# Kernel tuning notes

Measured on AMD Instinct MI355X. Metric: run time of the kernel, lower is better.

The kernel has to match this reference:

```python
import jax, jax.numpy as jnp
import numpy as np

BN_EPS = 1e-5
DIST_EPS = 1e-8
K = 3  # fixed 3-NN interpolation


def _cond_conv(x, t_embed, w_t, b_t, w_c, b_c, gamma, beta):
    # time conditioning: GELU(t) -> Linear -> add to channels
    te = jax.nn.gelu(t_embed, approximate=False) @ w_t.T + b_t  # (B, Cin)
    x = x + te[:, :, None]
    # kernel-size-1 Conv1d == channel GEMM
    x = jnp.einsum('oc,bcn->bon', w_c, x) + b_c[None, :, None]
    # BatchNorm1d, training mode: biased stats over (batch, length)
    m = jnp.mean(x, axis=(0, 2), keepdims=True)
    v = jnp.var(x, axis=(0, 2), keepdims=True)
    x = gamma[None, :, None] * (x - m) * jax.lax.rsqrt(v + BN_EPS) + beta[None, :, None]
    return jax.nn.gelu(x, approximate=False)


def _forward(xyz1, xyz2, points1, points2, t_embed,
             w_t1, b_t1, w_c1, b_c1, g1, be1,
             w_t2, b_t2, w_c2, b_c2, g2, be2):
    # squared euclidean distances (cdist**2), computed directly
    # d2[b,n,s] = ||xyz1[b,n]||^2 + ||xyz2[b,s]||^2 - 2 <xyz1[b,n], xyz2[b,s]>
    n1 = jnp.sum(xyz1 * xyz1, axis=-1)  # (B,N)
    n2 = jnp.sum(xyz2 * xyz2, axis=-1)  # (B,S)
    d2 = n1[:, :, None] + n2[:, None, :] - 2.0 * jnp.einsum('bnc,bsc->bns', xyz1, xyz2)
    # top-3 smallest distances (instead of wasteful full sort)
    neg, idx = jax.lax.top_k(-d2, K)        # (B,N,3)
    dists = -neg
    dist_recip = 1.0 / (dists + DIST_EPS)
    weight = dist_recip / jnp.sum(dist_recip, axis=2, keepdims=True)  # (B,N,3)
    pts2t = jnp.transpose(points2, (0, 2, 1))  # (B,S,C2)
    gathered = jax.vmap(lambda p, i: p[i])(pts2t, idx)  # (B,N,3,C2)
    interp = jnp.einsum('bnkc,bnk->bcn', gathered, weight)  # (B,C2,N)
    new_points = jnp.concatenate([points1, interp], axis=1)  # (B,C1+C2,N)
    new_points = _cond_conv(new_points, t_embed, w_t1, b_t1, w_c1, b_c1, g1, be1)
    new_points = _cond_conv(new_points, t_embed, w_t2, b_t2, w_c2, b_c2, g2, be2)
    return new_points


def setup_inputs() -> dict:
    key = jax.random.key(0)
    ks = jax.random.split(key, 12)
    B, N, S, C1, C2, T = 8, 8192, 2048, 128, 256, 256
    Cin = C1 + C2
    s = lambda fan: 1.0 / np.sqrt(fan)
    return {
        'xyz1': jax.random.normal(ks[0], (B, N, 3), jnp.float32),
        'xyz2': jax.random.normal(ks[1], (B, S, 3), jnp.float32),
        'points1': jax.random.normal(ks[2], (B, C1, N), jnp.float32),
        'points2': jax.random.normal(ks[3], (B, C2, S), jnp.float32),
        't_embed': jax.random.normal(ks[4], (B, T), jnp.float32),
        'w_t1': jax.random.normal(ks[5], (Cin, T), jnp.float32) * s(T),
        'b_t1': jnp.zeros((Cin,), jnp.float32),
        'w_c1': jax.random.normal(ks[6], (256, Cin), jnp.float32) * s(Cin),
        'b_c1': jnp.zeros((256,), jnp.float32),
        'g1': jnp.ones((256,), jnp.float32),
        'be1': jnp.zeros((256,), jnp.float32),
        'w_t2': jax.random.normal(ks[7], (256, T), jnp.float32) * s(T),
        'b_t2': jnp.zeros((256,), jnp.float32),
        'w_c2': jax.random.normal(ks[8], (256, 256), jnp.float32) * s(256),
        'b_c2': jnp.zeros((256,), jnp.float32),
        'g2': jnp.ones((256,), jnp.float32),
        'be2': jnp.zeros((256,), jnp.float32),
    }


def reference(xyz1, xyz2, points1, points2, t_embed,
              w_t1, b_t1, w_c1, b_c1, g1, be1,
              w_t2, b_t2, w_c2, b_c2, g2, be2):
    return _forward(xyz1, xyz2, points1, points2, t_embed,
                    w_t1, b_t1, w_c1, b_c1, g1, be1,
                    w_t2, b_t2, w_c2, b_c2, g2, be2)
```

## Files before the change

kernel.cpp:

```cpp
#include <hip/hip_runtime.h>
#include <cfloat>
#include <cmath>

#define B_   8
#define N_   8192
#define S_   2048
#define C1_  128
#define C2_  256
#define T_   256
#define CIN_ 384
#define CO_  256

#define KCH  16
#define KCS  (S_ / KCH)
#define KQB  512

typedef __attribute__((ext_vector_type(8))) short short8;
typedef __attribute__((ext_vector_type(4))) float f32x4;

__device__ __forceinline__ float bf2f(unsigned short u) {
    union { unsigned int i; float f; } v; v.i = ((unsigned int)u) << 16; return v.f;
}
__device__ __forceinline__ unsigned short f2bf(float f) {
    union { float f; unsigned int i; } v; v.f = f;
    unsigned int i = v.i;
    unsigned int r = i + 0x7FFFu + ((i >> 16) & 1u);
    return (unsigned short)(r >> 16);
}
__device__ __forceinline__ float gelu_f(float x) {
    return 0.5f * x * (1.0f + erff(x * 0.70710678118654752440f));
}
__device__ __forceinline__ void async16(const void* g, void* l) {
    __builtin_amdgcn_global_load_lds((const __attribute__((address_space(1))) void*)g,
                                     (__attribute__((address_space(3))) void*)l, 16, 0, 0);
}

#define OFF_TE1   0u
#define OFF_TE2   16384u
#define OFF_BN1   28672u
#define OFF_BN2   30720u
#define OFF_IDX   32768u
#define OFF_WTS   819200u
#define OFF_WC1   1605632u
#define OFF_WC2   1802240u
#define OFF_P2T   2097152u
#define OFF_X1    10485760u
#define OFF_Y     60817408u
#define OFF_PD    OFF_X1
#define OFF_PI    (OFF_X1 + 12582912u)
#define OFF_PS    OFF_P2T
#define OFF_PQ    (OFF_P2T + 1048576u)

__global__ __launch_bounds__(256) void wcvt_kernel(
    const float* __restrict__ w1, const float* __restrict__ w2,
    unsigned short* __restrict__ o1, unsigned short* __restrict__ o2)
{
    int g = blockIdx.x * 256 + threadIdx.x;
    o1[g] = f2bf(w1[g]);
    if (g < CO_ * CO_) o2[g] = f2bf(w2[g]);
}

__global__ __launch_bounds__(640) void te_kernel(
    const float* __restrict__ t_embed,
    const float* __restrict__ w_t1, const float* __restrict__ b_t1,
    const float* __restrict__ w_t2, const float* __restrict__ b_t2,
    float* __restrict__ te1, float* __restrict__ te2)
{
    __shared__ float gt[T_];
    int b = blockIdx.x, t = threadIdx.x;
    if (t < T_) gt[t] = gelu_f(t_embed[b * T_ + t]);
    __syncthreads();
    if (t < CIN_) {
        const float* w = w_t1 + t * T_;
        float s = 0.f;
        for (int k = 0; k < T_; ++k) s += gt[k] * w[k];
        te1[b * CIN_ + t] = s + b_t1[t];
    } else {
        int o = t - CIN_;
        const float* w = w_t2 + o * T_;
        float s = 0.f;
        for (int k = 0; k < T_; ++k) s += gt[k] * w[k];
        te2[b * CO_ + o] = s + b_t2[o];
    }
}

__global__ __launch_bounds__(256) void knn_part_kernel(
    const float* __restrict__ xyz1, const float* __restrict__ xyz2,
    float* __restrict__ pd, int* __restrict__ pi)
{
    __shared__ float4 sp[KCS];
    int b = blockIdx.z, ch = blockIdx.y, tid = threadIdx.x;
    int s0 = ch * KCS;
    if (tid < KCS) {
        int gs = s0 + tid;
        float x = xyz2[(b * S_ + gs) * 3 + 0];
        float y = xyz2[(b * S_ + gs) * 3 + 1];
        float z = xyz2[(b * S_ + gs) * 3 + 2];
        sp[tid] = make_float4(x, y, z, x * x + y * y + z * z);
    }
    __syncthreads();

    float nx[2], ny[2], nz[2], nn[2];
    float d1[2], d2[2], d3[2];
    int   i1[2], i2[2], i3[2];
    #pragma unroll
    for (int qq = 0; qq < 2; ++qq) {
        int n = blockIdx.x * KQB + qq * 256 + tid;
        float x1 = xyz1[(b * N_ + n) * 3 + 0];
        float y1 = xyz1[(b * N_ + n) * 3 + 1];
        float z1 = xyz1[(b * N_ + n) * 3 + 2];
        nn[qq] = x1 * x1 + y1 * y1 + z1 * z1;
        nx[qq] = -2.0f * x1; ny[qq] = -2.0f * y1; nz[qq] = -2.0f * z1;
        d1[qq] = FLT_MAX; d2[qq] = FLT_MAX; d3[qq] = FLT_MAX;
        i1[qq] = 0; i2[qq] = 0; i3[qq] = 0;
    }

    for (int s = 0; s < KCS; s += 4) {
        #pragma unroll
        for (int u = 0; u < 4; ++u) {
            float4 p = sp[s + u];
            int gi = s0 + s + u;
            #pragma unroll
            for (int qq = 0; qq < 2; ++qq) {
                float d = fmaf(nx[qq], p.x,
                          fmaf(ny[qq], p.y,
                          fmaf(nz[qq], p.z, p.w)));
                bool c1 = d < d1[qq];
                bool c2 = d < d2[qq];
                bool c3 = d < d3[qq];
                float e1 = fminf(d1[qq], d);
                float e2 = __builtin_amdgcn_fmed3f(d1[qq], d2[qq], d);
                float e3 = __builtin_amdgcn_fmed3f(d2[qq], d3[qq], d);
                int u1  = c1 ? i1[qq] : gi;
                int n1i = c1 ? gi : i1[qq];
                int n2i = c2 ? u1 : i2[qq];
                int u2  = c2 ? i2[qq] : gi;
                int n3i = c3 ? u2 : i3[qq];
                d1[qq] = e1; d2[qq] = e2; d3[qq] = e3;
                i1[qq] = n1i; i2[qq] = n2i; i3[qq] = n3i;
            }
        }
    }

    #pragma unroll
    for (int qq = 0; qq < 2; ++qq) {
        int n = blockIdx.x * KQB + qq * 256 + tid;
        size_t pb = (((size_t)b * KCH + ch) * N_ + n) * 3;
        pd[pb + 0] = d1[qq] + nn[qq];
        pd[pb + 1] = d2[qq] + nn[qq];
        pd[pb + 2] = d3[qq] + nn[qq];
        pi[pb + 0] = i1[qq]; pi[pb + 1] = i2[qq]; pi[pb + 2] = i3[qq];
    }
}

__global__ __launch_bounds__(256) void knn_merge_kernel(
    const float* __restrict__ pd, const int* __restrict__ pi,
    int* __restrict__ idx, float* __restrict__ wts)
{
    int g = blockIdx.x * 256 + threadIdx.x;
    int b = g >> 13, n = g & (N_ - 1);
    float d1 = FLT_MAX, d2 = FLT_MAX, d3 = FLT_MAX;
    int   i1 = 0, i2 = 0, i3 = 0;
    for (int ch = 0; ch < KCH; ++ch) {
        size_t pb = (((size_t)b * KCH + ch) * N_ + n) * 3;
        #pragma unroll
        for (int k = 0; k < 3; ++k) {
            float d = pd[pb + k];
            int   s = pi[pb + k];
            if (d < d3) {
                if (d < d2) {
                    d3 = d2; i3 = i2;
                    if (d < d1) { d2 = d1; i2 = i1; d1 = d; i1 = s; }
                    else        { d2 = d;  i2 = s; }
                } else { d3 = d; i3 = s; }
            }
        }
    }
    float r1 = 1.0f / (d1 + 1e-8f);
    float r2 = 1.0f / (d2 + 1e-8f);
    float r3 = 1.0f / (d3 + 1e-8f);
    float rs = 1.0f / (r1 + r2 + r3);
    size_t base = (size_t)g * 3;
    idx[base] = i1; idx[base + 1] = i2; idx[base + 2] = i3;
    wts[base] = r1 * rs; wts[base + 1] = r2 * rs; wts[base + 2] = r3 * rs;
}

__global__ __launch_bounds__(256) void transpose_p2(
    const float* __restrict__ p2, unsigned short* __restrict__ p2t)
{
    __shared__ unsigned short tile[32][33];
    int b = blockIdx.z, s0 = blockIdx.x * 32, c0 = blockIdx.y * 32;
    #pragma unroll
    for (int j = 0; j < 4; ++j) {
        int c = threadIdx.y + j * 8;
        tile[c][threadIdx.x] = f2bf(p2[((size_t)b * C2_ + c0 + c) * S_ + s0 + threadIdx.x]);
    }
    __syncthreads();
    #pragma unroll
    for (int j = 0; j < 4; ++j) {
        int s = threadIdx.y + j * 8;
        p2t[((size_t)b * S_ + s0 + s) * C2_ + c0 + threadIdx.x] = tile[threadIdx.x][s];
    }
}

__global__ __launch_bounds__(256) void transpose_p1(
    const float* __restrict__ p1, const float* __restrict__ te1,
    unsigned short* __restrict__ X1)
{
    __shared__ unsigned short tile[32][33];
    int b = blockIdx.z, n0 = blockIdx.x * 32, c0 = blockIdx.y * 32;
    const float* te = te1 + b * CIN_;
    #pragma unroll
    for (int j = 0; j < 4; ++j) {
        int c = threadIdx.y + j * 8;
        tile[c][threadIdx.x] =
            f2bf(p1[((size_t)b * C1_ + c0 + c) * N_ + n0 + threadIdx.x] + te[c0 + c]);
    }
    __syncthreads();
    #pragma unroll
    for (int j = 0; j < 4; ++j) {
        int n = threadIdx.y + j * 8;
        X1[((size_t)b * N_ + n0 + n) * CIN_ + c0 + threadIdx.x] = tile[threadIdx.x][n];
    }
}

__global__ __launch_bounds__(256) void interp_kernel(
    const unsigned short* __restrict__ p2t,
    const int* __restrict__ idx, const float* __restrict__ wts,
    const float* __restrict__ te1, unsigned short* __restrict__ X1)
{
    __shared__ float ste[C2_];
    int tid = threadIdx.x;
    int b = blockIdx.x >> 10;
    ste[tid] = te1[b * CIN_ + C1_ + tid];
    __syncthreads();
    int half = tid >> 5;
    int chunk = tid & 31;
    int gr = blockIdx.x * 8 + half;
    size_t base3 = (size_t)gr * 3;
    int j0 = idx[base3], j1 = idx[base3 + 1], j2 = idx[base3 + 2];
    float w0 = wts[base3], w1 = wts[base3 + 1], w2 = wts[base3 + 2];
    int co = chunk * 8;
    const unsigned short* r0 = p2t + ((size_t)b * S_ + j0) * C2_ + co;
    const unsigned short* r1 = p2t + ((size_t)b * S_ + j1) * C2_ + co;
    const unsigned short* r2 = p2t + ((size_t)b * S_ + j2) * C2_ + co;
    union { short8 v; unsigned short u[8]; } a0, a1, a2, pk;
    a0.v = *(const short8*)r0;
    a1.v = *(const short8*)r1;
    a2.v = *(const short8*)r2;
    #pragma unroll
    for (int jj = 0; jj < 8; ++jj) {
        float v = w0 * bf2f(a0.u[jj]) + w1 * bf2f(a1.u[jj]) + w2 * bf2f(a2.u[jj])
                + ste[co + jj];
        pk.u[jj] = f2bf(v);
    }
    *(short8*)&X1[(size_t)gr * CIN_ + C1_ + co] = pk.v;
}

template <int K, int MODE>
__global__ __launch_bounds__(256) void gemm_bt(
    const unsigned short* __restrict__ A,
    const unsigned short* __restrict__ X,
    const float* __restrict__ bias,
    unsigned short* __restrict__ out,
    float* __restrict__ psum, float* __restrict__ psq)
{
    __shared__ unsigned short sA[128 * 64];
    __shared__ unsigned short sB[128 * 64];
    const int tid = threadIdx.x;
    const int lane = tid & 63, wave = tid >> 6;
    const int wo = wave >> 1, wm = wave & 1;
    const int quad = lane >> 4, col = lane & 15;
    const int b = blockIdx.z;
    const int x = blockIdx.x;
    const int perm = (x & 7) * 16 + (x >> 3);
    const int n_t = perm >> 1, o_t = perm & 1;
    const int o0 = o_t * 128;
    const int n0 = n_t * 128;
    const unsigned short* Xb = X + (size_t)b * N_ * K;
    const int prow = ((b << 6) + n_t) * 2 + wm;

    f32x4 acc[4][4];
    #pragma unroll
    for (int i = 0; i < 4; ++i)
        #pragma unroll
        for (int j = 0; j < 4; ++j) acc[i][j] = (f32x4){0.f, 0.f, 0.f, 0.f};

    for (int k0 = 0; k0 < K; k0 += 64) {
        #pragma unroll
        for (int i = 0; i < 4; ++i) {
            int chunk = i * 256 + tid;
            int row = chunk >> 3, c8 = chunk & 7;
            async16(&A [(o0 + row) * K + k0 + c8 * 8], &sA[chunk * 8]);
            async16(&Xb[(size_t)(n0 + row) * K + k0 + c8 * 8], &sB[chunk * 8]);
        }
        __syncthreads();
        #pragma unroll
        for (int kk = 0; kk < 64; kk += 32) {
            short8 af[4], bfr[4];
            #pragma unroll
            for (int i = 0; i < 4; ++i)
                af[i] = *(const short8*)&sA[(wo * 64 + i * 16 + col) * 64 + kk + quad * 8];
            #pragma unroll
            for (int j = 0; j < 4; ++j)
                bfr[j] = *(const short8*)&sB[(wm * 64 + j * 16 + col) * 64 + kk + quad * 8];
            #pragma unroll
            for (int i = 0; i < 4; ++i)
                #pragma unroll
                for (int j = 0; j < 4; ++j)
                    acc[i][j] = __builtin_amdgcn_mfma_f32_16x16x32_bf16(af[i], bfr[j], acc[i][j], 0, 0, 0);
        }
        __syncthreads();
    }

    #pragma unroll
    for (int i = 0; i < 4; ++i) {
        int oo = o0 + wo * 64 + i * 16 + quad * 4;
        float bv0 = bias[oo + 0], bv1 = bias[oo + 1];
        float bv2 = bias[oo + 2], bv3 = bias[oo + 3];
        float s0 = 0.f, s1 = 0.f, s2 = 0.f, s3 = 0.f;
        float q0 = 0.f, q1 = 0.f, q2 = 0.f, q3 = 0.f;
        #pragma unroll
        for (int j = 0; j < 4; ++j) {
            int nn = n0 + wm * 64 + j * 16 + col;
            float v0 = acc[i][j][0] + bv0, v1 = acc[i][j][1] + bv1;
            float v2 = acc[i][j][2] + bv2, v3 = acc[i][j][3] + bv3;
            s0 += v0; q0 += v0 * v0; s1 += v1; q1 += v1 * v1;
            s2 += v2; q2 += v2 * v2; s3 += v3; q3 += v3 * v3;
            if (MODE == 0) {
                union { unsigned short u[4]; uint2 p; } pk;
                pk.u[0] = f2bf(v0); pk.u[1] = f2bf(v1);
                pk.u[2] = f2bf(v2); pk.u[3] = f2bf(v3);
                *(uint2*)&out[((size_t)b * N_ + nn) * CO_ + oo] = pk.p;
            } else {
                out[((size_t)b * CO_ + oo + 0) * N_ + nn] = f2bf(v0);
                out[((size_t)b * CO_ + oo + 1) * N_ + nn] = f2bf(v1);
                out[((size_t)b * CO_ + oo + 2) * N_ + nn] = f2bf(v2);
                out[((size_t)b * CO_ + oo + 3) * N_ + nn] = f2bf(v3);
            }
        }
        #pragma unroll
        for (int off = 1; off < 16; off <<= 1) {
            s0 += __shfl_down(s0, off); q0 += __shfl_down(q0, off);
            s1 += __shfl_down(s1, off); q1 += __shfl_down(q1, off);
            s2 += __shfl_down(s2, off); q2 += __shfl_down(q2, off);
            s3 += __shfl_down(s3, off); q3 += __shfl_down(q3, off);
        }
        if (col == 0) {
            float* ps = psum + (size_t)oo * 1024 + prow;
            float* pq = psq  + (size_t)oo * 1024 + prow;
            ps[0] = s0; ps[1024] = s1; ps[2048] = s2; ps[3072] = s3;
            pq[0] = q0; pq[1024] = q1; pq[2048] = q2; pq[3072] = q3;
        }
    }
}

__global__ __launch_bounds__(256) void bn_reduce_kernel(
    const float* __restrict__ psum, const float* __restrict__ psq,
    const float* __restrict__ gamma, const float* __restrict__ beta,
    float* __restrict__ scale, float* __restrict__ shift)
{
    int ch = blockIdx.x * 8 + (threadIdx.x >> 5);
    int l = threadIdx.x & 31;
    float s = 0.f, q = 0.f;
    for (int r = l; r < 1024; r += 32) {
        s += psum[(size_t)ch * 1024 + r];
        q += psq [(size_t)ch * 1024 + r];
    }
    #pragma unroll
    for (int off = 16; off > 0; off >>= 1) {
        s += __shfl_down(s, off, 32);
        q += __shfl_down(q, off, 32);
    }
    if (l == 0) {
        const float inv = 1.0f / 65536.0f;
        float m = s * inv;
        float var = fmaxf(q * inv - m * m, 0.f);
        float sc = gamma[ch] / sqrtf(var + 1e-5f);
        scale[ch] = sc;
        shift[ch] = beta[ch] - m * sc;
    }
}

__global__ __launch_bounds__(256) void apply1_kernel(
    unsigned short* __restrict__ y, const float* __restrict__ scale,
    const float* __restrict__ shift, const float* __restrict__ te2)
{
    __shared__ float ssc[CO_], ssh[CO_], ste[CO_];
    int b = blockIdx.x >> 10;
    int t = threadIdx.x;
    ssc[t] = scale[t]; ssh[t] = shift[t]; ste[t] = te2[b * CO_ + t];
    __syncthreads();
    int g = blockIdx.x * 256 + t;
    int row = g >> 5;
    int og = (g & 31) * 8;
    unsigned short* p = y + (size_t)row * CO_ + og;
    union { short8 v; unsigned short u[8]; } in, op;
    in.v = *(short8*)p;
    #pragma unroll
    for (int jj = 0; jj < 8; ++jj) {
        int o = og + jj;
        op.u[jj] = f2bf(gelu_f(ssc[o] * bf2f(in.u[jj]) + ssh[o]) + ste[o]);
    }
    *(short8*)p = op.v;
}

__global__ __launch_bounds__(256) void final_kernel(
    const unsigned short* __restrict__ z, const float* __restrict__ scale,
    const float* __restrict__ shift, float* __restrict__ out)
{
    int g = blockIdx.x * 256 + threadIdx.x;
    size_t e = (size_t)g * 8;
    int row = (int)(e >> 13);
    int o = row & (CO_ - 1);
    float sc = scale[o], sh = shift[o];
    union { short8 v; unsigned short u[8]; } in;
    in.v = *(const short8*)&z[e];
    float vo[8];
    #pragma unroll
    for (int jj = 0; jj < 8; ++jj)
        vo[jj] = gelu_f(sc * bf2f(in.u[jj]) + sh);
    *(float4*)&out[e]     = make_float4(vo[0], vo[1], vo[2], vo[3]);
    *(float4*)&out[e + 4] = make_float4(vo[4], vo[5], vo[6], vo[7]);
}

extern "C" void kernel_launch(void* const* d_in, const int* in_sizes, int n_in,
                              void* d_out, int out_size, void* d_ws, size_t ws_size,
                              hipStream_t stream)
{
    (void)in_sizes; (void)n_in; (void)out_size; (void)ws_size;
    const float* xyz1    = (const float*)d_in[0];
    const float* xyz2    = (const float*)d_in[1];
    const float* points1 = (const float*)d_in[2];
    const float* points2 = (const float*)d_in[3];
    const float* t_embed = (const float*)d_in[4];
    const float* w_t1    = (const float*)d_in[5];
    const float* b_t1    = (const float*)d_in[6];
    const float* w_c1    = (const float*)d_in[7];
    const float* b_c1    = (const float*)d_in[8];
    const float* g1      = (const float*)d_in[9];
    const float* be1     = (const float*)d_in[10];
    const float* w_t2    = (const float*)d_in[11];
    const float* b_t2    = (const float*)d_in[12];
    const float* w_c2    = (const float*)d_in[13];
    const float* b_c2    = (const float*)d_in[14];
    const float* g2      = (const float*)d_in[15];
    const float* be2     = (const float*)d_in[16];

    char* w = (char*)d_ws;
    float* te1        = (float*)(w + OFF_TE1);
    float* te2        = (float*)(w + OFF_TE2);
    float* scale1     = (float*)(w + OFF_BN1);
    float* shift1     = scale1 + 256;
    float* scale2     = (float*)(w + OFF_BN2);
    float* shift2     = scale2 + 256;
    int*   idx        = (int*)(w + OFF_IDX);
    float* wts        = (float*)(w + OFF_WTS);
    unsigned short* wc1 = (unsigned short*)(w + OFF_WC1);
    unsigned short* wc2 = (unsigned short*)(w + OFF_WC2);
    unsigned short* p2t = (unsigned short*)(w + OFF_P2T);
    float* pd         = (float*)(w + OFF_PD);
    int*   pi         = (int*)(w + OFF_PI);
    float* psum       = (float*)(w + OFF_PS);
    float* psq        = (float*)(w + OFF_PQ);
    unsigned short* X1  = (unsigned short*)(w + OFF_X1);
    unsigned short* Z   = (unsigned short*)(w + OFF_X1);
    unsigned short* Y   = (unsigned short*)(w + OFF_Y);
    float* out = (float*)d_out;

    hipLaunchKernelGGL(wcvt_kernel, dim3(CIN_ * CO_ / 256), dim3(256), 0, stream,
                       w_c1, w_c2, wc1, wc2);
    hipLaunchKernelGGL(te_kernel, dim3(B_), dim3(640), 0, stream,
                       t_embed, w_t1, b_t1, w_t2, b_t2, te1, te2);
    hipLaunchKernelGGL(knn_part_kernel, dim3(N_ / KQB, KCH, B_), dim3(256), 0, stream,
                       xyz1, xyz2, pd, pi);
    hipLaunchKernelGGL(knn_merge_kernel, dim3(B_ * N_ / 256), dim3(256), 0, stream,
                       pd, pi, idx, wts);
    hipLaunchKernelGGL(transpose_p2, dim3(S_ / 32, C2_ / 32, B_), dim3(32, 8), 0, stream,
                       points2, p2t);
    hipLaunchKernelGGL(transpose_p1, dim3(N_ / 32, C1_ / 32, B_), dim3(32, 8), 0, stream,
                       points1, te1, X1);
    hipLaunchKernelGGL(interp_kernel, dim3(B_ * N_ / 8), dim3(256), 0, stream,
                       p2t, idx, wts, te1, X1);
    hipLaunchKernelGGL((gemm_bt<CIN_, 0>), dim3(128, 1, B_), dim3(256), 0, stream,
                       wc1, X1, b_c1, Y, psum, psq);
    hipLaunchKernelGGL(bn_reduce_kernel, dim3(32), dim3(256), 0, stream,
                       psum, psq, g1, be1, scale1, shift1);
    hipLaunchKernelGGL(apply1_kernel, dim3(8192), dim3(256), 0, stream,
                       Y, scale1, shift1, te2);
    hipLaunchKernelGGL((gemm_bt<CO_, 1>), dim3(128, 1, B_), dim3(256), 0, stream,
                       wc2, Y, b_c2, Z, psum, psq);
    hipLaunchKernelGGL(bn_reduce_kernel, dim3(32), dim3(256), 0, stream,
                       psum, psq, g2, be2, scale2, shift2);
    hipLaunchKernelGGL(final_kernel, dim3(8192), dim3(256), 0, stream,
                       Z, scale2, shift2, out);
}
```

Before: 363.3 us.

## Fuse prep, transpose, and KNN merge into interpolation; widen KNN query tile

Merges weight conversion and time-embedding into one prep kernel and the two transposes into one launch. The separate KNN merge kernel is removed: the interpolation kernel now reduces the 16 partial top-3 lists per point with wave shuffles and computes the weights in place, so the idx/wts arrays no longer round-trip through global memory. Partial results move to the Y buffer so they don't collide with X1. The KNN part kernel now handles 4 queries per thread instead of 2, which adds register pressure and halves the number of blocks.

After: 347.5 us. 4.3% less time.

```diff
diff --git a/kernel.cpp b/kernel.cpp
--- a/kernel.cpp
+++ b/kernel.cpp
@@ -13,7 +13,7 @@
 
 #define KCH  16
 #define KCS  (S_ / KCH)
-#define KQB  512
+#define KQB  1024
 
 typedef __attribute__((ext_vector_type(8))) short short8;
 typedef __attribute__((ext_vector_type(4))) float f32x4;
@@ -39,48 +39,48 @@
 #define OFF_TE2   16384u
 #define OFF_BN1   28672u
 #define OFF_BN2   30720u
-#define OFF_IDX   32768u
-#define OFF_WTS   819200u
 #define OFF_WC1   1605632u
 #define OFF_WC2   1802240u
 #define OFF_P2T   2097152u
 #define OFF_X1    10485760u
 #define OFF_Y     60817408u
-#define OFF_PD    OFF_X1
-#define OFF_PI    (OFF_X1 + 12582912u)
+#define OFF_PD    OFF_Y
+#define OFF_PI    (OFF_Y + 12582912u)
 #define OFF_PS    OFF_P2T
 #define OFF_PQ    (OFF_P2T + 1048576u)
 
-__global__ __launch_bounds__(256) void wcvt_kernel(
+__global__ __launch_bounds__(256) void prep_kernel(
     const float* __restrict__ w1, const float* __restrict__ w2,
-    unsigned short* __restrict__ o1, unsigned short* __restrict__ o2)
-{
-    int g = blockIdx.x * 256 + threadIdx.x;
-    o1[g] = f2bf(w1[g]);
-    if (g < CO_ * CO_) o2[g] = f2bf(w2[g]);
-}
-
-__global__ __launch_bounds__(640) void te_kernel(
+    unsigned short* __restrict__ o1, unsigned short* __restrict__ o2,
     const float* __restrict__ t_embed,
     const float* __restrict__ w_t1, const float* __restrict__ b_t1,
     const float* __restrict__ w_t2, const float* __restrict__ b_t2,
     float* __restrict__ te1, float* __restrict__ te2)
 {
+    int bx = blockIdx.x, t = threadIdx.x;
+    if (bx < 384) {
+        int g = bx * 256 + t;
+        o1[g] = f2bf(w1[g]);
+        if (g < CO_ * CO_) o2[g] = f2bf(w2[g]);
+        return;
+    }
     __shared__ float gt[T_];
-    int b = blockIdx.x, t = threadIdx.x;
-    if (t < T_) gt[t] = gelu_f(t_embed[b * T_ + t]);
+    int b = bx - 384;
+    gt[t] = gelu_f(t_embed[b * T_ + t]);
     __syncthreads();
-    if (t < CIN_) {
-        const float* w = w_t1 + t * T_;
-        float s = 0.f;
-        for (int k = 0; k < T_; ++k) s += gt[k] * w[k];
-        te1[b * CIN_ + t] = s + b_t1[t];
-    } else {
-        int o = t - CIN_;
-        const float* w = w_t2 + o * T_;
-        float s = 0.f;
-        for (int k = 0; k < T_; ++k) s += gt[k] * w[k];
-        te2[b * CO_ + o] = s + b_t2[o];
+    for (int o = t; o < CIN_ + CO_; o += 256) {
+        if (o < CIN_) {
+            const float* w = w_t1 + o * T_;
+            float s = 0.f;
+            for (int k = 0; k < T_; ++k) s += gt[k] * w[k];
+            te1[b * CIN_ + o] = s + b_t1[o];
+        } else {
+            int oo = o - CIN_;
+            const float* w = w_t2 + oo * T_;
+            float s = 0.f;
+            for (int k = 0; k < T_; ++k) s += gt[k] * w[k];
+            te2[b * CO_ + oo] = s + b_t2[oo];
+        }
     }
 }
 
@@ -100,11 +100,11 @@
     }
     __syncthreads();
 
-    float nx[2], ny[2], nz[2], nn[2];
-    float d1[2], d2[2], d3[2];
-    int   i1[2], i2[2], i3[2];
-    #pragma unroll
-    for (int qq = 0; qq < 2; ++qq) {
+    float nx[4], ny[4], nz[4], nn[4];
+    float d1[4], d2[4], d3[4];
+    int   i1[4], i2[4], i3[4];
+    #pragma unroll
+    for (int qq = 0; qq < 4; ++qq) {
         int n = blockIdx.x * KQB + qq * 256 + tid;
         float x1 = xyz1[(b * N_ + n) * 3 + 0];
         float y1 = xyz1[(b * N_ + n) * 3 + 1];
@@ -121,7 +121,7 @@
             float4 p = sp[s + u];
             int gi = s0 + s + u;
             #pragma unroll
-            for (int qq = 0; qq < 2; ++qq) {
+            for (int qq = 0; qq < 4; ++qq) {
                 float d = fmaf(nx[qq], p.x,
                           fmaf(ny[qq], p.y,
                           fmaf(nz[qq], p.z, p.w)));
@@ -143,7 +143,7 @@
     }
 
     #pragma unroll
-    for (int qq = 0; qq < 2; ++qq) {
+    for (int qq = 0; qq < 4; ++qq) {
         int n = blockIdx.x * KQB + qq * 256 + tid;
         size_t pb = (((size_t)b * KCH + ch) * N_ + n) * 3;
         pd[pb + 0] = d1[qq] + nn[qq];
@@ -153,101 +153,118 @@
     }
 }
 
-__global__ __launch_bounds__(256) void knn_merge_kernel(
+__global__ __launch_bounds__(256) void transpose_fused(
+    const float* __restrict__ p2, unsigned short* __restrict__ p2t,
+    const float* __restrict__ p1, const float* __restrict__ te1,
+    unsigned short* __restrict__ X1)
+{
+    __shared__ unsigned short tile[32][33];
+    int bx = blockIdx.x;
+    if (bx < 4096) {
+        int b = bx >> 9, cy = (bx >> 6) & 7, sx = bx & 63;
+        int s0 = sx * 32, c0 = cy * 32;
+        #pragma unroll
+        for (int j = 0; j < 4; ++j) {
+            int c = threadIdx.y + j * 8;
+            tile[c][threadIdx.x] = f2bf(p2[((size_t)b * C2_ + c0 + c) * S_ + s0 + threadIdx.x]);
+        }
+        __syncthreads();
+        #pragma unroll
+        for (int j = 0; j < 4; ++j) {
+            int s = threadIdx.y + j * 8;
+            p2t[((size_t)b * S_ + s0 + s) * C2_ + c0 + threadIdx.x] = tile[threadIdx.x][s];
+        }
+    } else {
+        int bz = bx - 4096;
+        int b = bz >> 10, cy = (bz >> 8) & 3, nx = bz & 255;
+        int n0 = nx * 32, c0 = cy * 32;
+        const float* te = te1 + b * CIN_;
+        #pragma unroll
+        for (int j = 0; j < 4; ++j) {
+            int c = threadIdx.y + j * 8;
+            tile[c][threadIdx.x] =
+                f2bf(p1[((size_t)b * C1_ + c0 + c) * N_ + n0 + threadIdx.x] + te[c0 + c]);
+        }
+        __syncthreads();
+        #pragma unroll
+        for (int j = 0; j < 4; ++j) {
+            int n = threadIdx.y + j * 8;
+            X1[((size_t)b * N_ + n0 + n) * CIN_ + c0 + threadIdx.x] = tile[threadIdx.x][n];
+        }
+    }
+}
+
+__global__ __launch_bounds__(256) void interp2_kernel(
     const float* __restrict__ pd, const int* __restrict__ pi,
-    int* __restrict__ idx, float* __restrict__ wts)
-{
-    int g = blockIdx.x * 256 + threadIdx.x;
-    int b = g >> 13, n = g & (N_ - 1);
-    float d1 = FLT_MAX, d2 = FLT_MAX, d3 = FLT_MAX;
-    int   i1 = 0, i2 = 0, i3 = 0;
-    for (int ch = 0; ch < KCH; ++ch) {
-        size_t pb = (((size_t)b * KCH + ch) * N_ + n) * 3;
+    const unsigned short* __restrict__ p2t,
+    const float* __restrict__ te1, unsigned short* __restrict__ X1)
+{
+    __shared__ float spd[KCH][8][3];
+    __shared__ int   spi[KCH][8][3];
+    __shared__ float ste[C2_];
+    int tid = threadIdx.x;
+    int b = blockIdx.x >> 10;
+    int n0 = (blockIdx.x & 1023) * 8;
+    ste[tid] = te1[b * CIN_ + C1_ + tid];
+    if (tid < 128) {
+        int ch = tid >> 3, r = tid & 7;
+        size_t pb = (((size_t)b * KCH + ch) * N_ + n0 + r) * 3;
+        spd[ch][r][0] = pd[pb]; spd[ch][r][1] = pd[pb + 1]; spd[ch][r][2] = pd[pb + 2];
+    } else {
+        int t2 = tid - 128;
+        int ch = t2 >> 3, r = t2 & 7;
+        size_t pb = (((size_t)b * KCH + ch) * N_ + n0 + r) * 3;
+        spi[ch][r][0] = pi[pb]; spi[ch][r][1] = pi[pb + 1]; spi[ch][r][2] = pi[pb + 2];
+    }
+    __syncthreads();
+
+    int r = tid >> 5;
+    int l = tid & 31;
+    float d1, d2, d3; int i1, i2, i3;
+    if (l < KCH) {
+        d1 = spd[l][r][0]; d2 = spd[l][r][1]; d3 = spd[l][r][2];
+        i1 = spi[l][r][0]; i2 = spi[l][r][1]; i3 = spi[l][r][2];
+    } else {
+        d1 = d2 = d3 = FLT_MAX;
+        i1 = i2 = i3 = 0x7FFFFFFF;
+    }
+    #pragma unroll
+    for (int m = 1; m <= 8; m <<= 1) {
+        float pd1 = __shfl_xor(d1, m), pd2 = __shfl_xor(d2, m), pd3 = __shfl_xor(d3, m);
+        int   pi1 = __shfl_xor(i1, m), pi2 = __shfl_xor(i2, m), pi3 = __shfl_xor(i3, m);
         #pragma unroll
         for (int k = 0; k < 3; ++k) {
-            float d = pd[pb + k];
-            int   s = pi[pb + k];
-            if (d < d3) {
-                if (d < d2) {
-                    d3 = d2; i3 = i2;
-                    if (d < d1) { d2 = d1; i2 = i1; d1 = d; i1 = s; }
-                    else        { d2 = d;  i2 = s; }
-                } else { d3 = d; i3 = s; }
-            }
-        }
-    }
+            float d = (k == 0) ? pd1 : (k == 1) ? pd2 : pd3;
+            int   i = (k == 0) ? pi1 : (k == 1) ? pi2 : pi3;
+            bool c1 = (d < d1) || (d == d1 && i < i1);
+            bool c2 = (d < d2) || (d == d2 && i < i2);
+            bool c3 = (d < d3) || (d == d3 && i < i3);
+            float e1 = c1 ? d : d1;        int j1 = c1 ? i : i1;
+            float e2 = c1 ? d1 : (c2 ? d : d2);
+            int   j2 = c1 ? i1 : (c2 ? i : i2);
+            float e3 = c2 ? d2 : (c3 ? d : d3);
+            int   j3 = c2 ? i2 : (c3 ? i : i3);
+            d1 = e1; d2 = e2; d3 = e3; i1 = j1; i2 = j2; i3 = j3;
+        }
+    }
+    int base = threadIdx.x & 32;
+    d1 = __shfl(d1, base); d2 = __shfl(d2, base); d3 = __shfl(d3, base);
+    i1 = __shfl(i1, base); i2 = __shfl(i2, base); i3 = __shfl(i3, base);
     float r1 = 1.0f / (d1 + 1e-8f);
     float r2 = 1.0f / (d2 + 1e-8f);
     float r3 = 1.0f / (d3 + 1e-8f);
     float rs = 1.0f / (r1 + r2 + r3);
-    size_t base = (size_t)g * 3;
-    idx[base] = i1; idx[base + 1] = i2; idx[base + 2] = i3;
-    wts[base] = r1 * rs; wts[base + 1] = r2 * rs; wts[base + 2] = r3 * rs;
-}
-
-__global__ __launch_bounds__(256) void transpose_p2(
-    const float* __restrict__ p2, unsigned short* __restrict__ p2t)
-{
-    __shared__ unsigned short tile[32][33];
-    int b = blockIdx.z, s0 = blockIdx.x * 32, c0 = blockIdx.y * 32;
-    #pragma unroll
-    for (int j = 0; j < 4; ++j) {
-        int c = threadIdx.y + j * 8;
-        tile[c][threadIdx.x] = f2bf(p2[((size_t)b * C2_ + c0 + c) * S_ + s0 + threadIdx.x]);
-    }
-    __syncthreads();
-    #pragma unroll
-    for (int j = 0; j < 4; ++j) {
-        int s = threadIdx.y + j * 8;
-        p2t[((size_t)b * S_ + s0 + s) * C2_ + c0 + threadIdx.x] = tile[threadIdx.x][s];
-    }
-}
-
-__global__ __launch_bounds__(256) void transpose_p1(
-    const float* __restrict__ p1, const float* __restrict__ te1,
-    unsigned short* __restrict__ X1)
-{
-    __shared__ unsigned short tile[32][33];
-    int b = blockIdx.z, n0 = blockIdx.x * 32, c0 = blockIdx.y * 32;
-    const float* te = te1 + b * CIN_;
-    #pragma unroll
-    for (int j = 0; j < 4; ++j) {
-        int c = threadIdx.y + j * 8;
-        tile[c][threadIdx.x] =
-            f2bf(p1[((size_t)b * C1_ + c0 + c) * N_ + n0 + threadIdx.x] + te[c0 + c]);
-    }
-    __syncthreads();
-    #pragma unroll
-    for (int j = 0; j < 4; ++j) {
-        int n = threadIdx.y + j * 8;
-        X1[((size_t)b * N_ + n0 + n) * CIN_ + c0 + threadIdx.x] = tile[threadIdx.x][n];
-    }
-}
-
-__global__ __launch_bounds__(256) void interp_kernel(
-    const unsigned short* __restrict__ p2t,
-    const int* __restrict__ idx, const float* __restrict__ wts,
-    const float* __restrict__ te1, unsigned short* __restrict__ X1)
-{
-    __shared__ float ste[C2_];
-    int tid = threadIdx.x;
-    int b = blockIdx.x >> 10;
-    ste[tid] = te1[b * CIN_ + C1_ + tid];
-    __syncthreads();
-    int half = tid >> 5;
-    int chunk = tid & 31;
-    int gr = blockIdx.x * 8 + half;
-    size_t base3 = (size_t)gr * 3;
-    int j0 = idx[base3], j1 = idx[base3 + 1], j2 = idx[base3 + 2];
-    float w0 = wts[base3], w1 = wts[base3 + 1], w2 = wts[base3 + 2];
-    int co = chunk * 8;
-    const unsigned short* r0 = p2t + ((size_t)b * S_ + j0) * C2_ + co;
-    const unsigned short* r1 = p2t + ((size_t)b * S_ + j1) * C2_ + co;
-    const unsigned short* r2 = p2t + ((size_t)b * S_ + j2) * C2_ + co;
+    float w0 = r1 * rs, w1 = r2 * rs, w2 = r3 * rs;
+
+    int gr = (b << 13) + n0 + r;
+    int co = l * 8;
+    const unsigned short* q0 = p2t + ((size_t)b * S_ + i1) * C2_ + co;
+    const unsigned short* q1 = p2t + ((size_t)b * S_ + i2) * C2_ + co;
+    const unsigned short* q2 = p2t + ((size_t)b * S_ + i3) * C2_ + co;
     union { short8 v; unsigned short u[8]; } a0, a1, a2, pk;
-    a0.v = *(const short8*)r0;
-    a1.v = *(const short8*)r1;
-    a2.v = *(const short8*)r2;
+    a0.v = *(const short8*)q0;
+    a1.v = *(const short8*)q1;
+    a2.v = *(const short8*)q2;
     #pragma unroll
     for (int jj = 0; jj < 8; ++jj) {
         float v = w0 * bf2f(a0.u[jj]) + w1 * bf2f(a1.u[jj]) + w2 * bf2f(a2.u[jj])
@@ -454,8 +471,6 @@
     float* shift1     = scale1 + 256;
     float* scale2     = (float*)(w + OFF_BN2);
     float* shift2     = scale2 + 256;
-    int*   idx        = (int*)(w + OFF_IDX);
-    float* wts        = (float*)(w + OFF_WTS);
     unsigned short* wc1 = (unsigned short*)(w + OFF_WC1);
     unsigned short* wc2 = (unsigned short*)(w + OFF_WC2);
     unsigned short* p2t = (unsigned short*)(w + OFF_P2T);
@@ -468,20 +483,14 @@
     unsigned short* Y   = (unsigned short*)(w + OFF_Y);
     float* out = (float*)d_out;
 
-    hipLaunchKernelGGL(wcvt_kernel, dim3(CIN_ * CO_ / 256), dim3(256), 0, stream,
-                       w_c1, w_c2, wc1, wc2);
-    hipLaunchKernelGGL(te_kernel, dim3(B_), dim3(640), 0, stream,
-                       t_embed, w_t1, b_t1, w_t2, b_t2, te1, te2);
+    hipLaunchKernelGGL(prep_kernel, dim3(392), dim3(256), 0, stream,
+                       w_c1, w_c2, wc1, wc2, t_embed, w_t1, b_t1, w_t2, b_t2, te1, te2);
     hipLaunchKernelGGL(knn_part_kernel, dim3(N_ / KQB, KCH, B_), dim3(256), 0, stream,
                        xyz1, xyz2, pd, pi);
-    hipLaunchKernelGGL(knn_merge_kernel, dim3(B_ * N_ / 256), dim3(256), 0, stream,
-                       pd, pi, idx, wts);
-    hipLaunchKernelGGL(transpose_p2, dim3(S_ / 32, C2_ / 32, B_), dim3(32, 8), 0, stream,
-                       points2, p2t);
-    hipLaunchKernelGGL(transpose_p1, dim3(N_ / 32, C1_ / 32, B_), dim3(32, 8), 0, stream,
-                       points1, te1, X1);
-    hipLaunchKernelGGL(interp_kernel, dim3(B_ * N_ / 8), dim3(256), 0, stream,
-                       p2t, idx, wts, te1, X1);
+    hipLaunchKernelGGL(transpose_fused, dim3(12288), dim3(32, 8), 0, stream,
+                       points2, p2t, points1, te1, X1);
+    hipLaunchKernelGGL(interp2_kernel, dim3(B_ * N_ / 8), dim3(256), 0, stream,
+                       pd, pi, p2t, te1, X1);
     hipLaunchKernelGGL((gemm_bt<CIN_, 0>), dim3(128, 1, B_), dim3(256), 0, stream,
                        wc1, X1, b_c1, Y, psum, psq);
     hipLaunchKernelGGL(bn_reduce_kernel, dim3(32), dim3(256), 0, stream,
```
